# Kernel tuning notes

Hardware: AMD Instinct MI355X
Metric: run time of the kernel (lower is better)

## Reference

```python
import jax, jax.numpy as jnp
import numpy as np

NUM_HEADS = 12
LN_EPS = 1e-5


def _layernorm(x, w, b):
    m = jnp.mean(x, axis=-1, keepdims=True)
    v = jnp.mean(jnp.square(x - m), axis=-1, keepdims=True)
    return (x - m) * jax.lax.rsqrt(v + LN_EPS) * w + b


def setup_inputs() -> dict:
    key = jax.random.key(0)
    ks = jax.random.split(key, 6)
    B, N, C, H = 8, 1024, 768, 3072
    s = 0.02
    return {
        "x": jax.random.normal(ks[0], (B, N, C), jnp.float32),
        "ln1_w": jnp.ones((C,), jnp.float32),
        "ln1_b": jnp.zeros((C,), jnp.float32),
        "qkv_w": jax.random.normal(ks[1], (3 * C, C), jnp.float32) * s,
        "qkv_b": jnp.zeros((3 * C,), jnp.float32),
        "proj_w": jax.random.normal(ks[2], (C, C), jnp.float32) * s,
        "proj_b": jnp.zeros((C,), jnp.float32),
        "ln2_w": jnp.ones((C,), jnp.float32),
        "ln2_b": jnp.zeros((C,), jnp.float32),
        "fc1_w": jax.random.normal(ks[3], (H, C), jnp.float32) * s,
        "fc1_b": jnp.zeros((H,), jnp.float32),
        "fc2_w": jax.random.normal(ks[4], (C, H), jnp.float32) * s,
        "fc2_b": jnp.zeros((C,), jnp.float32),
    }


def reference(x, ln1_w, ln1_b, qkv_w, qkv_b, proj_w, proj_b,
              ln2_w, ln2_b, fc1_w, fc1_b, fc2_w, fc2_b):
    B, N, C = x.shape
    H = NUM_HEADS
    d = C // H
    scale = d ** (-0.5)

    # --- attention on norm1(x) (size=None path, dropout rates are 0) ---
    h = _layernorm(x, ln1_w, ln1_b)
    qkv = h @ qkv_w.T + qkv_b                      # [B,N,3C]
    qkv = qkv.reshape(B, N, 3, H, d).transpose(2, 0, 3, 1, 4)  # [3,B,H,N,d]
    q, k, v = qkv[0], qkv[1], qkv[2]
    attn = jnp.einsum('bhqd,bhkd->bhqk', q, k) * scale
    attn = jax.nn.softmax(attn, axis=-1)
    o = jnp.einsum('bhqk,bhkd->bhqd', attn, v)     # [B,H,N,d]
    o = o.transpose(0, 2, 1, 3).reshape(B, N, C)
    x_attn = o @ proj_w.T + proj_b

    # --- residual + MLP ---
    x = x + x_attn
    h2 = _layernorm(x, ln2_w, ln2_b)
    h2 = jax.nn.gelu(h2 @ fc1_w.T + fc1_b, approximate=False)
    x = x + (h2 @ fc2_w.T + fc2_b)
    return x
```

## Files before the change

kernel.cpp:

```cpp
#include <hip/hip_runtime.h>
#include <cmath>

typedef __bf16 bf16;
typedef __bf16 bf16x8 __attribute__((ext_vector_type(8)));
typedef __bf16 bf16x4 __attribute__((ext_vector_type(4)));
typedef float floatx4 __attribute__((ext_vector_type(4)));

#define MFMA16(A, B, C) __builtin_amdgcn_mfma_f32_16x16x32_bf16((A), (B), (C), 0, 0, 0)

#define GLDS16(g, l)                                                   \
  __builtin_amdgcn_global_load_lds(                                    \
      (const __attribute__((address_space(1))) void*)(g),              \
      (__attribute__((address_space(3))) void*)(l), 16, 0, 0)

__global__ __launch_bounds__(256) void f2b_kernel(const float* __restrict__ s,
                                                  bf16* __restrict__ d, int n4) {
  int i = blockIdx.x * 256 + threadIdx.x;
  if (i < n4) {
    const float* p = s + (size_t)i * 4;
    bf16x4 v;
    v[0] = (bf16)p[0];
    v[1] = (bf16)p[1];
    v[2] = (bf16)p[2];
    v[3] = (bf16)p[3];
    *(bf16x4*)(d + (size_t)i * 4) = v;
  }
}

__global__ __launch_bounds__(256) void ln_kernel(const float* __restrict__ x,
                                                 const float* __restrict__ g,
                                                 const float* __restrict__ be,
                                                 bf16* __restrict__ out) {
  int row = blockIdx.x;
  int t = threadIdx.x;
  const float* xr = x + (size_t)row * 768;
  float v0 = xr[t], v1 = xr[t + 256], v2 = xr[t + 512];
  float s = v0 + v1 + v2;
  float s2 = v0 * v0 + v1 * v1 + v2 * v2;
#pragma unroll
  for (int o = 1; o < 64; o <<= 1) {
    s += __shfl_xor(s, o, 64);
    s2 += __shfl_xor(s2, o, 64);
  }
  __shared__ float red[8];
  int w = t >> 6, lane = t & 63;
  if (lane == 0) { red[w] = s; red[4 + w] = s2; }
  __syncthreads();
  float ts = red[0] + red[1] + red[2] + red[3];
  float ts2 = red[4] + red[5] + red[6] + red[7];
  float mean = ts * (1.0f / 768.0f);
  float var = ts2 * (1.0f / 768.0f) - mean * mean;
  float rstd = rsqrtf(var + 1e-5f);
  bf16* orow = out + (size_t)row * 768;
  orow[t]       = (bf16)((v0 - mean) * rstd * g[t]       + be[t]);
  orow[t + 256] = (bf16)((v1 - mean) * rstd * g[t + 256] + be[t + 256]);
  orow[t + 512] = (bf16)((v2 - mean) * rstd * g[t + 512] + be[t + 512]);
}

constexpr int EP_BF16 = 0;
constexpr int EP_RES_F32 = 1;
constexpr int EP_GELU_BF16 = 2;

template <int EP>
__global__ __launch_bounds__(256, 3) void gemm_bt(
    const bf16* __restrict__ A, const bf16* __restrict__ Bw,
    const float* __restrict__ bias, const float* __restrict__ resid,
    void* __restrict__ outp, int M, int N, int K) {
  __shared__ alignas(16) bf16 Asl[128 * 32];
  __shared__ alignas(16) bf16 Bsl[128 * 32];
  int tid = threadIdx.x;
  int lane = tid & 63, w = tid >> 6;
  int wm = w >> 1, wn = w & 1;
  int q16 = lane & 15, quad = lane >> 4;
  int m0 = blockIdx.y * 128, n0 = blockIdx.x * 128;
  floatx4 acc[4][4];
#pragma unroll
  for (int i = 0; i < 4; i++)
#pragma unroll
    for (int j = 0; j < 4; j++) acc[i][j] = (floatx4){0.f, 0.f, 0.f, 0.f};

  int rA = (lane >> 2), c8 = (lane & 3) * 8;
  const bf16* a0 = A + (size_t)(m0 + (w * 2 + 0) * 16 + rA) * K + c8;
  const bf16* a1 = A + (size_t)(m0 + (w * 2 + 1) * 16 + rA) * K + c8;
  const bf16* b0 = Bw + (size_t)(n0 + (w * 2 + 0) * 16 + rA) * K + c8;
  const bf16* b1 = Bw + (size_t)(n0 + (w * 2 + 1) * 16 + rA) * K + c8;
  bf16* la0 = &Asl[w * 1024];
  bf16* la1 = &Asl[w * 1024 + 512];
  bf16* lb0 = &Bsl[w * 1024];
  bf16* lb1 = &Bsl[w * 1024 + 512];

  for (int k0 = 0; k0 < K; k0 += 32) {
    __syncthreads();
    GLDS16(a0, la0);
    GLDS16(a1, la1);
    GLDS16(b0, lb0);
    GLDS16(b1, lb1);
    a0 += 32; a1 += 32; b0 += 32; b1 += 32;
    __syncthreads();
    bf16x8 af[4], bfr[4];
#pragma unroll
    for (int i = 0; i < 4; i++)
      af[i] = *(const bf16x8*)&Asl[(wm * 64 + i * 16 + q16) * 32 + quad * 8];
#pragma unroll
    for (int j = 0; j < 4; j++)
      bfr[j] = *(const bf16x8*)&Bsl[(wn * 64 + j * 16 + q16) * 32 + quad * 8];
#pragma unroll
    for (int i = 0; i < 4; i++)
#pragma unroll
      for (int j = 0; j < 4; j++) acc[i][j] = MFMA16(af[i], bfr[j], acc[i][j]);
  }

#pragma unroll
  for (int i = 0; i < 4; i++) {
#pragma unroll
    for (int j = 0; j < 4; j++) {
#pragma unroll
      for (int r = 0; r < 4; r++) {
        int m = m0 + wm * 64 + i * 16 + quad * 4 + r;
        int n = n0 + wn * 64 + j * 16 + q16;
        float v = acc[i][j][r] + bias[n];
        size_t idx = (size_t)m * N + n;
        if constexpr (EP == EP_BF16) {
          ((bf16*)outp)[idx] = (bf16)v;
        } else if constexpr (EP == EP_RES_F32) {
          ((float*)outp)[idx] = v + resid[idx];
        } else {
          float gv = 0.5f * v * (1.0f + erff(v * 0.70710678118654752f));
          ((bf16*)outp)[idx] = (bf16)gv;
        }
      }
    }
  }
}

__global__ __launch_bounds__(256, 3) void attn_kernel(const bf16* __restrict__ qkv,
                                                      bf16* __restrict__ o) {
  __shared__ alignas(16) bf16 Kl[32 * 64];
  __shared__ alignas(16) bf16 Vt[64 * 5 * 8];
  __shared__ alignas(16) bf16 Pl[4][2][16 * 40];
  int tid = threadIdx.x;
  int lane = tid & 63, w = tid >> 6;
  int q16 = lane & 15, quad = lane >> 4;
  int b = blockIdx.y / 12, h = blockIdx.y % 12;
  int qbase = blockIdx.x * 128 + w * 32;

  bf16x8 qf[2][2];
#pragma unroll
  for (int qt = 0; qt < 2; qt++)
#pragma unroll
    for (int c = 0; c < 2; c++)
      qf[qt][c] = *(const bf16x8*)(qkv +
          (size_t)(b * 1024 + qbase + qt * 16 + q16) * 2304 + h * 64 +
          c * 32 + quad * 8);

  int kkey = w * 8 + (lane >> 3);
  int kchunk = (lane & 7) ^ (lane >> 3);
  const bf16* kg = qkv + (size_t)(b * 1024 + kkey) * 2304 + 768 + h * 64 +
                   (kchunk & 7) * 8;
  bf16* kl_dst = &Kl[w * 512];

  int kr = tid >> 3;
  int kcb = (tid & 7) * 8;
  const bf16* vg = qkv + (size_t)(b * 1024 + kr) * 2304 + 1536 + h * 64 + kcb;
  int vt_idx[8];
#pragma unroll
  for (int e = 0; e < 8; e++)
    vt_idx[e] = ((((kcb + e) * 5) + w) ^ (tid & 7)) * 8 + (kr & 7);

  int koff[2][2];
#pragma unroll
  for (int nc = 0; nc < 2; nc++)
#pragma unroll
    for (int ck = 0; ck < 2; ck++) {
      int key = nc * 16 + q16;
      koff[nc][ck] = (key * 8 + ((ck * 4 + quad) ^ (key & 7))) * 8;
    }
  int voff[4];
#pragma unroll
  for (int dc = 0; dc < 4; dc++) {
    int d = dc * 16 + q16;
    voff[dc] = ((d * 5 + quad) ^ ((d >> 3) & 7)) * 8;
  }
  const bf16* pread = &Pl[w][0][q16 * 40 + quad * 8];
  int pw_base = (quad * 4) * 40 + q16;

  float l_[2][4];
  floatx4 oacc[2][4];
#pragma unroll
  for (int qt = 0; qt < 2; qt++)
#pragma unroll
    for (int r = 0; r < 4; r++) l_[qt][r] = 0.f;
#pragma unroll
  for (int qt = 0; qt < 2; qt++)
#pragma unroll
    for (int dc = 0; dc < 4; dc++) oacc[qt][dc] = (floatx4){0.f, 0.f, 0.f, 0.f};

  for (int kt = 0; kt < 32; kt++) {
    __syncthreads();
    GLDS16(kg, kl_dst);
    bf16x8 vv = *(const bf16x8*)vg;
    kg += 32 * 2304;
    vg += 32 * 2304;
#pragma unroll
    for (int e = 0; e < 8; e++) Vt[vt_idx[e]] = vv[e];
    __syncthreads();

    bf16x8 kf[2][2];
#pragma unroll
    for (int nc = 0; nc < 2; nc++)
#pragma unroll
      for (int ck = 0; ck < 2; ck++)
        kf[nc][ck] = *(const bf16x8*)&Kl[koff[nc][ck]];

#pragma unroll
    for (int qt = 0; qt < 2; qt++) {
#pragma unroll
      for (int nc = 0; nc < 2; nc++) {
        floatx4 z = (floatx4){0.f, 0.f, 0.f, 0.f};
        z = MFMA16(qf[qt][0], kf[nc][0], z);
        z = MFMA16(qf[qt][1], kf[nc][1], z);
#pragma unroll
        for (int r = 0; r < 4; r++) {
          float p = __builtin_amdgcn_exp2f(z[r] * 0.18033688011f);
          l_[qt][r] += p;
          Pl[w][qt][pw_base + r * 40 + nc * 16] = (bf16)p;
        }
      }
    }
    __syncthreads();

    bf16x8 vf[4];
#pragma unroll
    for (int dc = 0; dc < 4; dc++) vf[dc] = *(const bf16x8*)&Vt[voff[dc]];
#pragma unroll
    for (int qt = 0; qt < 2; qt++) {
      bf16x8 pf = *(const bf16x8*)(pread + qt * 640);
#pragma unroll
      for (int dc = 0; dc < 4; dc++)
        oacc[qt][dc] = MFMA16(pf, vf[dc], oacc[qt][dc]);
    }
  }

#pragma unroll
  for (int qt = 0; qt < 2; qt++) {
    bf16* op = o + (size_t)(b * 1024 + qbase + qt * 16) * 768 + h * 64;
#pragma unroll
    for (int r = 0; r < 4; r++) {
      float s = l_[qt][r];
#pragma unroll
      for (int off = 1; off < 16; off <<= 1) s += __shfl_xor(s, off, 16);
      float inv = 1.0f / s;
#pragma unroll
      for (int dc = 0; dc < 4; dc++)
        op[(size_t)(quad * 4 + r) * 768 + dc * 16 + q16] =
            (bf16)(oacc[qt][dc][r] * inv);
    }
  }
}

extern "C" void kernel_launch(void* const* d_in, const int* in_sizes, int n_in,
                              void* d_out, int out_size, void* d_ws, size_t ws_size,
                              hipStream_t stream) {
  (void)in_sizes; (void)n_in; (void)out_size; (void)ws_size;
  const float* x      = (const float*)d_in[0];
  const float* ln1_w  = (const float*)d_in[1];
  const float* ln1_b  = (const float*)d_in[2];
  const float* qkv_w  = (const float*)d_in[3];
  const float* qkv_b  = (const float*)d_in[4];
  const float* proj_w = (const float*)d_in[5];
  const float* proj_b = (const float*)d_in[6];
  const float* ln2_w  = (const float*)d_in[7];
  const float* ln2_b  = (const float*)d_in[8];
  const float* fc1_w  = (const float*)d_in[9];
  const float* fc1_b  = (const float*)d_in[10];
  const float* fc2_w  = (const float*)d_in[11];
  const float* fc2_b  = (const float*)d_in[12];

  char* ws = (char*)d_ws;
  size_t off = 0;
  auto alloc = [&](size_t bytes) {
    void* p = ws + off;
    off += (bytes + 255) & ~(size_t)255;
    return p;
  };
  bf16* wq  = (bf16*)alloc((size_t)2304 * 768 * 2);
  bf16* wp  = (bf16*)alloc((size_t)768 * 768 * 2);
  bf16* wf1 = (bf16*)alloc((size_t)3072 * 768 * 2);
  bf16* wf2 = (bf16*)alloc((size_t)768 * 3072 * 2);
  bf16* slotA = (bf16*)alloc((size_t)8192 * 768 * 2);
  bf16* slotB = (bf16*)alloc((size_t)8192 * 3072 * 2);
  float* x1 = (float*)alloc((size_t)8192 * 768 * 4);

  bf16* h1 = slotA;
  bf16* qkvb = slotB;
  bf16* ob = slotA;
  bf16* h2 = slotA;
  bf16* hm = slotB;

  f2b_kernel<<<(2304 * 768 / 4 + 255) / 256, 256, 0, stream>>>(qkv_w, wq, 2304 * 768 / 4);
  f2b_kernel<<<(768 * 768 / 4 + 255) / 256, 256, 0, stream>>>(proj_w, wp, 768 * 768 / 4);
  f2b_kernel<<<(3072 * 768 / 4 + 255) / 256, 256, 0, stream>>>(fc1_w, wf1, 3072 * 768 / 4);
  f2b_kernel<<<(768 * 3072 / 4 + 255) / 256, 256, 0, stream>>>(fc2_w, wf2, 768 * 3072 / 4);

  ln_kernel<<<8192, 256, 0, stream>>>(x, ln1_w, ln1_b, h1);
  gemm_bt<EP_BF16><<<dim3(18, 64), 256, 0, stream>>>(h1, wq, qkv_b, nullptr, qkvb,
                                                     8192, 2304, 768);
  attn_kernel<<<dim3(8, 96), 256, 0, stream>>>(qkvb, ob);
  gemm_bt<EP_RES_F32><<<dim3(6, 64), 256, 0, stream>>>(ob, wp, proj_b, x, x1,
                                                       8192, 768, 768);
  ln_kernel<<<8192, 256, 0, stream>>>(x1, ln2_w, ln2_b, h2);
  gemm_bt<EP_GELU_BF16><<<dim3(24, 64), 256, 0, stream>>>(h2, wf1, fc1_b, nullptr, hm,
                                                          8192, 3072, 768);
  gemm_bt<EP_RES_F32><<<dim3(6, 64), 256, 0, stream>>>(hm, wf2, fc2_b, x1,
                                                       (float*)d_out, 8192, 768, 3072);
}
```

Before: 398.7 us.

## Split-K the N=768 GEMMs and fuse reduction with residual and LayerNorm

The two narrow GEMMs (proj and fc2, N=768) now use split-K with two K slices, writing bf16 partials that a separate kernel sums. The proj reduction is fused with bias, residual and the second LayerNorm, which removes a standalone LN pass. Block indices are remapped into groups of eight M-panels to improve L2 reuse, and the four weight-conversion launches are merged into one. The cost is extra partial-sum traffic, and storing the partials in bf16 loses some accuracy.

After: 372.6 us. 6.6% less time.

```diff
diff --git a/kernel.cpp b/kernel.cpp
--- a/kernel.cpp
+++ b/kernel.cpp
@@ -13,18 +13,22 @@
       (const __attribute__((address_space(1))) void*)(g),              \
       (__attribute__((address_space(3))) void*)(l), 16, 0, 0)
 
-__global__ __launch_bounds__(256) void f2b_kernel(const float* __restrict__ s,
-                                                  bf16* __restrict__ d, int n4) {
+__global__ __launch_bounds__(256) void f2b4_kernel(
+    const float* __restrict__ s0, bf16* __restrict__ d0, int n0,
+    const float* __restrict__ s1, bf16* __restrict__ d1, int n1,
+    const float* __restrict__ s2, bf16* __restrict__ d2, int n2,
+    const float* __restrict__ s3, bf16* __restrict__ d3, int n3) {
   int i = blockIdx.x * 256 + threadIdx.x;
-  if (i < n4) {
-    const float* p = s + (size_t)i * 4;
-    bf16x4 v;
-    v[0] = (bf16)p[0];
-    v[1] = (bf16)p[1];
-    v[2] = (bf16)p[2];
-    v[3] = (bf16)p[3];
-    *(bf16x4*)(d + (size_t)i * 4) = v;
-  }
+  const float* s;
+  bf16* d;
+  if (i < n0) { s = s0 + (size_t)i * 4; d = d0 + (size_t)i * 4; }
+  else if ((i -= n0) < n1) { s = s1 + (size_t)i * 4; d = d1 + (size_t)i * 4; }
+  else if ((i -= n1) < n2) { s = s2 + (size_t)i * 4; d = d2 + (size_t)i * 4; }
+  else if ((i -= n2) < n3) { s = s3 + (size_t)i * 4; d = d3 + (size_t)i * 4; }
+  else return;
+  bf16x4 v;
+  v[0] = (bf16)s[0]; v[1] = (bf16)s[1]; v[2] = (bf16)s[2]; v[3] = (bf16)s[3];
+  *(bf16x4*)d = v;
 }
 
 __global__ __launch_bounds__(256) void ln_kernel(const float* __restrict__ x,
@@ -57,14 +61,68 @@
   orow[t + 512] = (bf16)((v2 - mean) * rstd * g[t + 512] + be[t + 512]);
 }
 
+__global__ __launch_bounds__(256) void reduce_ln_kernel(
+    const bf16* __restrict__ pp, const float* __restrict__ bias,
+    const float* __restrict__ x, const float* __restrict__ g,
+    const float* __restrict__ be, float* __restrict__ x1,
+    bf16* __restrict__ h2) {
+  int row = blockIdx.x;
+  int t = threadIdx.x;
+  const bf16* p0 = pp + (size_t)row * 768;
+  const bf16* p1 = pp + (size_t)(8192 + row) * 768;
+  const float* xr = x + (size_t)row * 768;
+  float v0 = (float)p0[t]       + (float)p1[t]       + bias[t]       + xr[t];
+  float v1 = (float)p0[t + 256] + (float)p1[t + 256] + bias[t + 256] + xr[t + 256];
+  float v2 = (float)p0[t + 512] + (float)p1[t + 512] + bias[t + 512] + xr[t + 512];
+  float* x1r = x1 + (size_t)row * 768;
+  x1r[t] = v0; x1r[t + 256] = v1; x1r[t + 512] = v2;
+  float s = v0 + v1 + v2;
+  float s2 = v0 * v0 + v1 * v1 + v2 * v2;
+#pragma unroll
+  for (int o = 1; o < 64; o <<= 1) {
+    s += __shfl_xor(s, o, 64);
+    s2 += __shfl_xor(s2, o, 64);
+  }
+  __shared__ float red[8];
+  int w = t >> 6, lane = t & 63;
+  if (lane == 0) { red[w] = s; red[4 + w] = s2; }
+  __syncthreads();
+  float ts = red[0] + red[1] + red[2] + red[3];
+  float ts2 = red[4] + red[5] + red[6] + red[7];
+  float mean = ts * (1.0f / 768.0f);
+  float var = ts2 * (1.0f / 768.0f) - mean * mean;
+  float rstd = rsqrtf(var + 1e-5f);
+  bf16* orow = h2 + (size_t)row * 768;
+  orow[t]       = (bf16)((v0 - mean) * rstd * g[t]       + be[t]);
+  orow[t + 256] = (bf16)((v1 - mean) * rstd * g[t + 256] + be[t + 256]);
+  orow[t + 512] = (bf16)((v2 - mean) * rstd * g[t + 512] + be[t + 512]);
+}
+
+__global__ __launch_bounds__(256) void reduce_out_kernel(
+    const bf16* __restrict__ pp, const float* __restrict__ bias,
+    const float* __restrict__ x1, float* __restrict__ out) {
+  int i = blockIdx.x * 256 + threadIdx.x;
+  size_t base = (size_t)i * 4;
+  int col = (int)(base % 768);
+  bf16x4 a = *(const bf16x4*)(pp + base);
+  bf16x4 b = *(const bf16x4*)(pp + (size_t)8192 * 768 + base);
+  float4 xr = *(const float4*)(x1 + base);
+  float4 r;
+  r.x = (float)a[0] + (float)b[0] + bias[col]     + xr.x;
+  r.y = (float)a[1] + (float)b[1] + bias[col + 1] + xr.y;
+  r.z = (float)a[2] + (float)b[2] + bias[col + 2] + xr.z;
+  r.w = (float)a[3] + (float)b[3] + bias[col + 3] + xr.w;
+  *(float4*)(out + base) = r;
+}
+
 constexpr int EP_BF16 = 0;
-constexpr int EP_RES_F32 = 1;
+constexpr int EP_PART = 1;
 constexpr int EP_GELU_BF16 = 2;
 
 template <int EP>
 __global__ __launch_bounds__(256, 3) void gemm_bt(
     const bf16* __restrict__ A, const bf16* __restrict__ Bw,
-    const float* __restrict__ bias, const float* __restrict__ resid,
+    const float* __restrict__ bias,
     void* __restrict__ outp, int M, int N, int K) {
   __shared__ alignas(16) bf16 Asl[128 * 32];
   __shared__ alignas(16) bf16 Bsl[128 * 32];
@@ -72,7 +130,15 @@
   int lane = tid & 63, w = tid >> 6;
   int wm = w >> 1, wn = w & 1;
   int q16 = lane & 15, quad = lane >> 4;
-  int m0 = blockIdx.y * 128, n0 = blockIdx.x * 128;
+  int fid = blockIdx.x + gridDim.x * blockIdx.y;
+  int nb = gridDim.x;
+  int s = fid >> 3;
+  int m0 = ((fid & 7) * (gridDim.y >> 3) + s / nb) * 128;
+  int n0 = (s % nb) * 128;
+  int kz = blockIdx.z;
+  int Ksub = K / gridDim.z;
+  int kbeg = kz * Ksub;
+
   floatx4 acc[4][4];
 #pragma unroll
   for (int i = 0; i < 4; i++)
@@ -80,16 +146,16 @@
     for (int j = 0; j < 4; j++) acc[i][j] = (floatx4){0.f, 0.f, 0.f, 0.f};
 
   int rA = (lane >> 2), c8 = (lane & 3) * 8;
-  const bf16* a0 = A + (size_t)(m0 + (w * 2 + 0) * 16 + rA) * K + c8;
-  const bf16* a1 = A + (size_t)(m0 + (w * 2 + 1) * 16 + rA) * K + c8;
-  const bf16* b0 = Bw + (size_t)(n0 + (w * 2 + 0) * 16 + rA) * K + c8;
-  const bf16* b1 = Bw + (size_t)(n0 + (w * 2 + 1) * 16 + rA) * K + c8;
+  const bf16* a0 = A + (size_t)(m0 + (w * 2 + 0) * 16 + rA) * K + kbeg + c8;
+  const bf16* a1 = A + (size_t)(m0 + (w * 2 + 1) * 16 + rA) * K + kbeg + c8;
+  const bf16* b0 = Bw + (size_t)(n0 + (w * 2 + 0) * 16 + rA) * K + kbeg + c8;
+  const bf16* b1 = Bw + (size_t)(n0 + (w * 2 + 1) * 16 + rA) * K + kbeg + c8;
   bf16* la0 = &Asl[w * 1024];
   bf16* la1 = &Asl[w * 1024 + 512];
   bf16* lb0 = &Bsl[w * 1024];
   bf16* lb1 = &Bsl[w * 1024 + 512];
 
-  for (int k0 = 0; k0 < K; k0 += 32) {
+  for (int k0 = 0; k0 < Ksub; k0 += 32) {
     __syncthreads();
     GLDS16(a0, la0);
     GLDS16(a1, la1);
@@ -110,6 +176,7 @@
       for (int j = 0; j < 4; j++) acc[i][j] = MFMA16(af[i], bfr[j], acc[i][j]);
   }
 
+  bf16* opart = (bf16*)outp + (size_t)kz * M * N;
 #pragma unroll
   for (int i = 0; i < 4; i++) {
 #pragma unroll
@@ -118,15 +185,17 @@
       for (int r = 0; r < 4; r++) {
         int m = m0 + wm * 64 + i * 16 + quad * 4 + r;
         int n = n0 + wn * 64 + j * 16 + q16;
-        float v = acc[i][j][r] + bias[n];
         size_t idx = (size_t)m * N + n;
-        if constexpr (EP == EP_BF16) {
-          ((bf16*)outp)[idx] = (bf16)v;
-        } else if constexpr (EP == EP_RES_F32) {
-          ((float*)outp)[idx] = v + resid[idx];
+        if constexpr (EP == EP_PART) {
+          opart[idx] = (bf16)acc[i][j][r];
         } else {
-          float gv = 0.5f * v * (1.0f + erff(v * 0.70710678118654752f));
-          ((bf16*)outp)[idx] = (bf16)gv;
+          float v = acc[i][j][r] + bias[n];
+          if constexpr (EP == EP_BF16) {
+            ((bf16*)outp)[idx] = (bf16)v;
+          } else {
+            float gv = 0.5f * v * (1.0f + erff(v * 0.70710678118654752f));
+            ((bf16*)outp)[idx] = (bf16)gv;
+          }
         }
       }
     }
@@ -290,6 +359,7 @@
   bf16* slotA = (bf16*)alloc((size_t)8192 * 768 * 2);
   bf16* slotB = (bf16*)alloc((size_t)8192 * 3072 * 2);
   float* x1 = (float*)alloc((size_t)8192 * 768 * 4);
+  bf16* part = (bf16*)alloc((size_t)2 * 8192 * 768 * 2);
 
   bf16* h1 = slotA;
   bf16* qkvb = slotB;
@@ -297,20 +367,21 @@
   bf16* h2 = slotA;
   bf16* hm = slotB;
 
-  f2b_kernel<<<(2304 * 768 / 4 + 255) / 256, 256, 0, stream>>>(qkv_w, wq, 2304 * 768 / 4);
-  f2b_kernel<<<(768 * 768 / 4 + 255) / 256, 256, 0, stream>>>(proj_w, wp, 768 * 768 / 4);
-  f2b_kernel<<<(3072 * 768 / 4 + 255) / 256, 256, 0, stream>>>(fc1_w, wf1, 3072 * 768 / 4);
-  f2b_kernel<<<(768 * 3072 / 4 + 255) / 256, 256, 0, stream>>>(fc2_w, wf2, 768 * 3072 / 4);
+  f2b4_kernel<<<6912, 256, 0, stream>>>(
+      qkv_w, wq, 2304 * 768 / 4, proj_w, wp, 768 * 768 / 4,
+      fc1_w, wf1, 3072 * 768 / 4, fc2_w, wf2, 768 * 3072 / 4);
 
   ln_kernel<<<8192, 256, 0, stream>>>(x, ln1_w, ln1_b, h1);
-  gemm_bt<EP_BF16><<<dim3(18, 64), 256, 0, stream>>>(h1, wq, qkv_b, nullptr, qkvb,
-                                                     8192, 2304, 768);
+  gemm_bt<EP_BF16><<<dim3(18, 64, 1), 256, 0, stream>>>(h1, wq, qkv_b, qkvb,
+                                                        8192, 2304, 768);
   attn_kernel<<<dim3(8, 96), 256, 0, stream>>>(qkvb, ob);
-  gemm_bt<EP_RES_F32><<<dim3(6, 64), 256, 0, stream>>>(ob, wp, proj_b, x, x1,
+  gemm_bt<EP_PART><<<dim3(6, 64, 2), 256, 0, stream>>>(ob, wp, nullptr, part,
                                                        8192, 768, 768);
-  ln_kernel<<<8192, 256, 0, stream>>>(x1, ln2_w, ln2_b, h2);
-  gemm_bt<EP_GELU_BF16><<<dim3(24, 64), 256, 0, stream>>>(h2, wf1, fc1_b, nullptr, hm,
-                                                          8192, 3072, 768);
-  gemm_bt<EP_RES_F32><<<dim3(6, 64), 256, 0, stream>>>(hm, wf2, fc2_b, x1,
-                                                       (float*)d_out, 8192, 768, 3072);
-}
+  reduce_ln_kernel<<<8192, 256, 0, stream>>>(part, proj_b, x, ln2_w, ln2_b,
+                                             x1, h2);
+  gemm_bt<EP_GELU_BF16><<<dim3(24, 64, 1), 256, 0, stream>>>(h2, wf1, fc1_b, hm,
+                                                             8192, 3072, 768);
+  gemm_bt<EP_PART><<<dim3(6, 64, 2), 256, 0, stream>>>(hm, wf2, nullptr, part,
+                                                       8192, 768, 3072);
+  reduce_out_kernel<<<6144, 256, 0, stream>>>(part, fc2_b, x1, (float*)d_out);
+}
```
